# Optimization experiments

Hardware: AMD Instinct MI355X
Metric: run time of the kernel (lower is better)

## Reference

```python
import jax, jax.numpy as jnp
import numpy as np

NUM_MODULES, INP, OUT = 64, 256, 256
B, T = 2048, 64


def setup_inputs() -> dict:
    key = jax.random.key(0)
    k1, k2, k3, k4 = jax.random.split(key, 4)
    x = jax.random.normal(k1, (B, T, INP), dtype=jnp.float32)
    indices = jax.random.randint(k2, (B,), 0, NUM_MODULES)
    # torch.nn.Linear init: U(-1/sqrt(in), 1/sqrt(in)) for both weight and bias
    bound = 1.0 / np.sqrt(INP)
    W = jax.random.uniform(k3, (NUM_MODULES, OUT, INP), minval=-bound, maxval=bound, dtype=jnp.float32)
    b = jax.random.uniform(k4, (NUM_MODULES, OUT), minval=-bound, maxval=bound, dtype=jnp.float32)
    return {"x": x, "indices": indices, "W": W, "b": b}


def reference(x, indices, W, b):
    # Per-sample expert selection: gather each sample's weight/bias, batched matmul.
    Wg = W[indices]            # [B, OUT, INP]
    bg = b[indices]            # [B, OUT]
    y = jnp.einsum("bti,boi->bto", x, Wg) + bg[:, None, :]
    return y
```

## Files before the change

kernel.cpp:

```cpp
#include <hip/hip_runtime.h>
#include <hip/hip_bf16.h>

#define NMOD 64
#define INPD 256
#define OUTD 256
#define BATCH 2048
#define TT 64
#define SPB 4

typedef __attribute__((ext_vector_type(8))) short short8;
typedef __attribute__((ext_vector_type(4))) float floatx4;

__device__ __forceinline__ unsigned int pack2(float a, float b) {
    union { float f; unsigned int u; } ua, ub; ua.f = a; ub.f = b;
    unsigned int ra = ua.u + 0x7fffu + ((ua.u >> 16) & 1u);
    unsigned int rb = ub.u + 0x7fffu + ((ub.u >> 16) & 1u);
    return (ra >> 16) | (rb & 0xffff0000u);
}

__global__ __launch_bounds__(256) void conv_w_kernel(const float* __restrict__ W,
                                                     uint4* __restrict__ Wp) {
    int gid  = blockIdx.x * 256 + threadIdx.x;
    int lane = gid & 63;
    int frag = (gid >> 6) & 15;
    int ks   = (gid >> 10) & 7;
    int e    = gid >> 13;

    int n = (frag >> 3) * 128 + (frag & 7) * 16 + (lane & 15);
    int k = ks * 32 + (lane >> 4) * 8;

    const float* p = W + ((size_t)e * OUTD + n) * INPD + k;
    float4 v0 = *reinterpret_cast<const float4*>(p);
    float4 v1 = *reinterpret_cast<const float4*>(p + 4);
    Wp[gid] = make_uint4(pack2(v0.x, v0.y), pack2(v0.z, v0.w),
                         pack2(v1.x, v1.y), pack2(v1.z, v1.w));
}

template <bool PRECONV>
__global__ __launch_bounds__(256, 3) void moe_gemm_kernel(
    const float* __restrict__ x, const int* __restrict__ idx,
    const void* __restrict__ Wsrc, const float* __restrict__ bias,
    float* __restrict__ y) {

    __shared__ unsigned short lx[2][4 * 4 * 64 * 8];

    const int bid  = blockIdx.x;
    const int s0   = bid * SPB;
    const int tid  = threadIdx.x;
    const int lane = tid & 63;
    const int w    = tid >> 6;
    const int l15  = lane & 15;
    const int kq   = lane >> 4;

    int e4[SPB];
#pragma unroll
    for (int i = 0; i < SPB; ++i) e4[i] = idx[s0 + i];

    char* const lb0 = reinterpret_cast<char*>(lx[0]);
    char* const lb1 = reinterpret_cast<char*>(lx[1]);

    auto stage_load = [&](int s, int h, float4* sv) {
        const float* xb = x + ((size_t)(s0 + s) * TT + w * 16 + l15) * INPD + kq * 8;
#pragma unroll
        for (int r = 0; r < 4; ++r) {
            const float* p = xb + (h * 4 + r) * 32;
            sv[2 * r]     = *reinterpret_cast<const float4*>(p);
            sv[2 * r + 1] = *reinterpret_cast<const float4*>(p + 4);
        }
    };
    auto stage_write = [&](char* lc, const float4* sv) {
#pragma unroll
        for (int r = 0; r < 4; ++r) {
            float4 a = sv[2 * r], c = sv[2 * r + 1];
            *reinterpret_cast<uint4*>(lc + ((((r * 4 + w) * 64) + lane) << 4)) =
                make_uint4(pack2(a.x, a.y), pack2(a.z, a.w),
                           pack2(c.x, c.y), pack2(c.z, c.w));
        }
    };

    floatx4 acc[4][4] = {};
    float4 sv[8];

    stage_load(0, 0, sv);
    stage_write(lb0, sv);
    __syncthreads();

#pragma unroll
    for (int t = 0; t < 2 * SPB; ++t) {
        const int s = t >> 1;
        const int h = t & 1;
        const int e = e4[s];

        if (t < 2 * SPB - 1)
            stage_load((t + 1) >> 1, (t + 1) & 1, sv);

        char* lc = (t & 1) ? lb1 : lb0;
        const unsigned short* wp0 = nullptr;
        const float* Wf = nullptr;
        if (PRECONV) {
            wp0 = reinterpret_cast<const unsigned short*>(Wsrc)
                  + ((size_t)e << 16) + (w << 11) + (lane << 3);
        } else {
            Wf = reinterpret_cast<const float*>(Wsrc) + (size_t)e * OUTD * INPD;
        }

#pragma unroll
        for (int kk = 0; kk < 4; ++kk) {
            const int ks = h * 4 + kk;

            short8 af[4];
#pragma unroll
            for (int mi = 0; mi < 4; ++mi)
                af[mi] = *reinterpret_cast<const short8*>(
                    lc + ((((kk * 4 + mi) * 64) + lane) << 4));

            short8 bf[4];
            if (PRECONV) {
                const unsigned short* wp = wp0 + ((size_t)ks << 13);
#pragma unroll
                for (int ni = 0; ni < 4; ++ni)
                    bf[ni] = *reinterpret_cast<const short8*>(wp + (ni << 9));
            } else {
#pragma unroll
                for (int ni = 0; ni < 4; ++ni) {
                    int n = w * 64 + ni * 16 + l15;
                    int k = ks * 32 + kq * 8;
                    const float* p = Wf + (size_t)n * INPD + k;
                    float4 v0 = *reinterpret_cast<const float4*>(p);
                    float4 v1 = *reinterpret_cast<const float4*>(p + 4);
                    union { short8 sh; uint4 u; } cv;
                    cv.u = make_uint4(pack2(v0.x, v0.y), pack2(v0.z, v0.w),
                                      pack2(v1.x, v1.y), pack2(v1.z, v1.w));
                    bf[ni] = cv.sh;
                }
            }

#pragma unroll
            for (int mi = 0; mi < 4; ++mi)
#pragma unroll
                for (int ni = 0; ni < 4; ++ni)
                    acc[mi][ni] = __builtin_amdgcn_mfma_f32_16x16x32_bf16(
                        bf[ni], af[mi], acc[mi][ni], 0, 0, 0);
        }

        if (t < 2 * SPB - 1)
            stage_write((t & 1) ? lb0 : lb1, sv);

        if (h == 1) {
            const floatx4* bp =
                reinterpret_cast<const floatx4*>(bias + e * OUTD + w * 64) + kq;
            floatx4 bv[4];
#pragma unroll
            for (int ni = 0; ni < 4; ++ni)
                bv[ni] = bp[ni * 4];

            float* yb = y + ((size_t)(s0 + s) * TT + l15) * OUTD + w * 64 + kq * 4;
#pragma unroll
            for (int mi = 0; mi < 4; ++mi) {
                float* yrow = yb + mi * (16 * OUTD);
#pragma unroll
                for (int ni = 0; ni < 4; ++ni) {
                    floatx4 out = acc[mi][ni] + bv[ni];
                    __builtin_nontemporal_store(
                        out, reinterpret_cast<floatx4*>(yrow + ni * 16));
                    acc[mi][ni] = (floatx4)0.0f;
                }
            }
        }

        if (t < 2 * SPB - 1)
            __syncthreads();
    }
}

extern "C" void kernel_launch(void* const* d_in, const int* in_sizes, int n_in,
                              void* d_out, int out_size, void* d_ws, size_t ws_size,
                              hipStream_t stream) {
    const float* x    = (const float*)d_in[0];
    const int*   idx  = (const int*)d_in[1];
    const float* W    = (const float*)d_in[2];
    const float* bias = (const float*)d_in[3];
    float*       y    = (float*)d_out;

    const size_t w_elems      = (size_t)NMOD * OUTD * INPD;
    const size_t w_bf16_bytes = w_elems * sizeof(unsigned short);

    if (ws_size >= w_bf16_bytes) {
        conv_w_kernel<<<(unsigned)(w_elems / 8 / 256), 256, 0, stream>>>(
            W, reinterpret_cast<uint4*>(d_ws));
        moe_gemm_kernel<true><<<BATCH / SPB, 256, 0, stream>>>(x, idx, d_ws, bias, y);
    } else {
        moe_gemm_kernel<false><<<BATCH / SPB, 256, 0, stream>>>(x, idx, (const void*)W, bias, y);
    }
}
```

Measured before the change: 88.04 us.

## Halve samples per block, split x staging into chunks, raise occupancy target

Cuts samples per block from 4 to 2, which doubles the grid, and raises the launch-bounds occupancy hint from 3 to 4 blocks per CU. The x prefetch is split into two half-size chunks interleaved with the MFMA k-steps, and A fragments are loaded one at a time rather than all four up front, both to reduce register pressure. The custom bf16 rounding is replaced with the HIP intrinsic, and output stores lose the nontemporal hint. Risks include more blocks each reloading W and the bias, and extra cache pollution from ordinary stores.

```diff
diff --git a/kernel.cpp b/kernel.cpp
--- a/kernel.cpp
+++ b/kernel.cpp
@@ -6,16 +6,15 @@
 #define OUTD 256
 #define BATCH 2048
 #define TT 64
-#define SPB 4
+#define SPB 2
 
 typedef __attribute__((ext_vector_type(8))) short short8;
 typedef __attribute__((ext_vector_type(4))) float floatx4;
 
 __device__ __forceinline__ unsigned int pack2(float a, float b) {
-    union { float f; unsigned int u; } ua, ub; ua.f = a; ub.f = b;
-    unsigned int ra = ua.u + 0x7fffu + ((ua.u >> 16) & 1u);
-    unsigned int rb = ub.u + 0x7fffu + ((ub.u >> 16) & 1u);
-    return (ra >> 16) | (rb & 0xffff0000u);
+    union { __hip_bfloat162 h; unsigned int u; } cv;
+    cv.h = __float22bfloat162_rn(make_float2(a, b));
+    return cv.u;
 }
 
 __global__ __launch_bounds__(256) void conv_w_kernel(const float* __restrict__ W,
@@ -37,7 +36,7 @@
 }
 
 template <bool PRECONV>
-__global__ __launch_bounds__(256, 3) void moe_gemm_kernel(
+__global__ __launch_bounds__(256, 4) void moe_gemm_kernel(
     const float* __restrict__ x, const int* __restrict__ idx,
     const void* __restrict__ Wsrc, const float* __restrict__ bias,
     float* __restrict__ y) {
@@ -52,49 +51,55 @@
     const int l15  = lane & 15;
     const int kq   = lane >> 4;
 
-    int e4[SPB];
+    int eArr[SPB];
 #pragma unroll
-    for (int i = 0; i < SPB; ++i) e4[i] = idx[s0 + i];
+    for (int i = 0; i < SPB; ++i) eArr[i] = idx[s0 + i];
 
     char* const lb0 = reinterpret_cast<char*>(lx[0]);
     char* const lb1 = reinterpret_cast<char*>(lx[1]);
 
-    auto stage_load = [&](int s, int h, float4* sv) {
-        const float* xb = x + ((size_t)(s0 + s) * TT + w * 16 + l15) * INPD + kq * 8;
+    const float* xb0 = x + ((size_t)s0 * TT + w * 16 + l15) * INPD + kq * 8;
+
+    auto load_chunk = [&](int s, int h, int c, float4* sv) {
 #pragma unroll
-        for (int r = 0; r < 4; ++r) {
-            const float* p = xb + (h * 4 + r) * 32;
-            sv[2 * r]     = *reinterpret_cast<const float4*>(p);
-            sv[2 * r + 1] = *reinterpret_cast<const float4*>(p + 4);
+        for (int r2 = 0; r2 < 2; ++r2) {
+            int r = c * 2 + r2;
+            const float* p = xb0 + (size_t)s * (TT * INPD) + (h * 4 + r) * 32;
+            sv[2 * r2]     = *reinterpret_cast<const float4*>(p);
+            sv[2 * r2 + 1] = *reinterpret_cast<const float4*>(p + 4);
         }
     };
-    auto stage_write = [&](char* lc, const float4* sv) {
+    auto write_chunk = [&](char* lc, int c, const float4* sv) {
 #pragma unroll
-        for (int r = 0; r < 4; ++r) {
-            float4 a = sv[2 * r], c = sv[2 * r + 1];
+        for (int r2 = 0; r2 < 2; ++r2) {
+            int r = c * 2 + r2;
+            float4 a = sv[2 * r2], b2 = sv[2 * r2 + 1];
             *reinterpret_cast<uint4*>(lc + ((((r * 4 + w) * 64) + lane) << 4)) =
                 make_uint4(pack2(a.x, a.y), pack2(a.z, a.w),
-                           pack2(c.x, c.y), pack2(c.z, c.w));
+                           pack2(b2.x, b2.y), pack2(b2.z, b2.w));
         }
     };
 
     floatx4 acc[4][4] = {};
-    float4 sv[8];
+    float4 sv[4];
 
-    stage_load(0, 0, sv);
-    stage_write(lb0, sv);
+    load_chunk(0, 0, 0, sv);
+    write_chunk(lb0, 0, sv);
+    load_chunk(0, 0, 1, sv);
+    write_chunk(lb0, 1, sv);
     __syncthreads();
 
 #pragma unroll
     for (int t = 0; t < 2 * SPB; ++t) {
         const int s = t >> 1;
         const int h = t & 1;
-        const int e = e4[s];
+        const int e = eArr[s];
+        char* const lc  = (t & 1) ? lb1 : lb0;
+        char* const ln  = (t & 1) ? lb0 : lb1;
+        const bool pre  = (t < 2 * SPB - 1);
+        const int  sn   = (t + 1) >> 1;
+        const int  hn   = (t + 1) & 1;
 
-        if (t < 2 * SPB - 1)
-            stage_load((t + 1) >> 1, (t + 1) & 1, sv);
-
-        char* lc = (t & 1) ? lb1 : lb0;
         const unsigned short* wp0 = nullptr;
         const float* Wf = nullptr;
         if (PRECONV) {
@@ -104,16 +109,8 @@
             Wf = reinterpret_cast<const float*>(Wsrc) + (size_t)e * OUTD * INPD;
         }
 
-#pragma unroll
-        for (int kk = 0; kk < 4; ++kk) {
+        auto compute_kk = [&](int kk) {
             const int ks = h * 4 + kk;
-
-            short8 af[4];
-#pragma unroll
-            for (int mi = 0; mi < 4; ++mi)
-                af[mi] = *reinterpret_cast<const short8*>(
-                    lc + ((((kk * 4 + mi) * 64) + lane) << 4));
-
             short8 bf[4];
             if (PRECONV) {
                 const unsigned short* wp = wp0 + ((size_t)ks << 13);
@@ -134,17 +131,27 @@
                     bf[ni] = cv.sh;
                 }
             }
-
 #pragma unroll
-            for (int mi = 0; mi < 4; ++mi)
+            for (int mi = 0; mi < 4; ++mi) {
+                short8 af = *reinterpret_cast<const short8*>(
+                    lc + ((((kk * 4 + mi) * 64) + lane) << 4));
 #pragma unroll
                 for (int ni = 0; ni < 4; ++ni)
                     acc[mi][ni] = __builtin_amdgcn_mfma_f32_16x16x32_bf16(
-                        bf[ni], af[mi], acc[mi][ni], 0, 0, 0);
+                        bf[ni], af, acc[mi][ni], 0, 0, 0);
+            }
+        };
+
+        if (pre) load_chunk(sn, hn, 0, sv);
+        compute_kk(0);
+        compute_kk(1);
+        if (pre) {
+            write_chunk(ln, 0, sv);
+            load_chunk(sn, hn, 1, sv);
         }
-
-        if (t < 2 * SPB - 1)
-            stage_write((t & 1) ? lb0 : lb1, sv);
+        compute_kk(2);
+        compute_kk(3);
+        if (pre) write_chunk(ln, 1, sv);
 
         if (h == 1) {
             const floatx4* bp =
@@ -160,16 +167,13 @@
                 float* yrow = yb + mi * (16 * OUTD);
 #pragma unroll
                 for (int ni = 0; ni < 4; ++ni) {
-                    floatx4 out = acc[mi][ni] + bv[ni];
-                    __builtin_nontemporal_store(
-                        out, reinterpret_cast<floatx4*>(yrow + ni * 16));
-                    acc[mi][ni] = (floatx4)0.0f;
+                    *reinterpret_cast<floatx4*>(yrow + ni * 16) = acc[mi][ni] + bv[ni];
+                    if (s + 1 < SPB) acc[mi][ni] = (floatx4)0.0f;
                 }
             }
         }
 
-        if (t < 2 * SPB - 1)
-            __syncthreads();
+        if (pre) __syncthreads();
     }
 }
 
```

Result: no change. 87.52 us (-0.6%).
